# Performance work log

Measured on AMD Instinct MI355X. Metric: run time of the kernel, lower is better.

Reference implementation:

```python
import jax, jax.numpy as jnp
import numpy as np

N, CIN, COUT, K, CSTYLE, H, W = 8, 512, 512, 3, 512, 64, 64
EPS = 1e-8
SQRT2 = 2.0 ** 0.5


def setup_inputs() -> dict:
    key = jax.random.key(0)
    ks = jax.random.split(key, 5)
    return {
        "x": jax.random.normal(ks[0], (N, CIN, H, W), jnp.float32),
        "style": jax.random.normal(ks[1], (N, CSTYLE), jnp.float32),
        "noise": jax.random.normal(ks[2], (N, 1, H, W), jnp.float32),
        "conv_weight": jax.random.normal(ks[3], (1, COUT, CIN, K, K), jnp.float32),
        "mod_weight": jax.random.normal(ks[4], (CIN, CSTYLE), jnp.float32) / np.float32(np.sqrt(CSTYLE)),
        "mod_bias": jnp.ones((CIN,), jnp.float32),
        "noise_weight": jnp.zeros((1,), jnp.float32),
        "act_bias": jnp.zeros((COUT,), jnp.float32),
    }


def reference(x, style, noise, conv_weight, mod_weight, mod_bias, noise_weight, act_bias):
    n = x.shape[0]
    # style modulation: linear(style) -> per-sample per-in-channel scale (style_bias=0)
    s = style @ mod_weight.T + mod_bias                       # (n, cin)
    # modulate shared weight (1, cout, cin, k, k) -> (n, cout, cin, k, k)
    w = conv_weight * s[:, None, :, None, None]
    # demodulate
    demod = jax.lax.rsqrt(jnp.sum(w * w, axis=(2, 3, 4)) + EPS)  # (n, cout)
    w = w * demod[:, :, None, None, None]
    # grouped conv: groups = batch
    w = w.reshape(n * COUT, CIN, K, K)
    xg = x.reshape(1, n * CIN, H, W)
    out = jax.lax.conv_general_dilated(
        xg, w,
        window_strides=(1, 1),
        padding=[(K // 2, K // 2), (K // 2, K // 2)],
        dimension_numbers=("NCHW", "OIHW", "NCHW"),
        feature_group_count=n,
    )
    out = out.reshape(n, COUT, H, W) * SQRT2
    # noise injection (scalar weight, broadcast noise)
    out = out + noise_weight[0] * noise
    # fused bias + leaky relu (slope 0.2)
    out = jax.nn.leaky_relu(out + act_bias[None, :, None, None], negative_slope=0.2)
    return out
```

## Files before the change

kernel.cpp:

```cpp
#include <hip/hip_runtime.h>
#include <hip/hip_bf16.h>
#include <stdint.h>


typedef __attribute__((ext_vector_type(8))) short short8;
typedef __attribute__((ext_vector_type(4))) float f32x4;
typedef __attribute__((ext_vector_type(4))) unsigned int uint4v;
typedef __attribute__((ext_vector_type(2))) unsigned int uint2v;

__device__ __forceinline__ unsigned short f2bf(float f) {
  unsigned u = __builtin_bit_cast(unsigned, f);
  u += 0x7FFFu + ((u >> 16) & 1u);
  return (unsigned short)(u >> 16);
}

__device__ __forceinline__ void g2l16(const void* g, void* l) {
  __builtin_amdgcn_global_load_lds(
      (const __attribute__((address_space(1))) void*)g,
      (__attribute__((address_space(3))) void*)l, 16, 0, 0);
}

__global__ void k_pre(const float* __restrict__ style, const float* __restrict__ mw,
                      const float* __restrict__ mb, const float* __restrict__ cw,
                      float* __restrict__ s_out, float* __restrict__ wsq) {
  int t = threadIdx.x;
  int b = blockIdx.x;
  if (b < 1024) {
    int wid = b * 4 + (t >> 6);
    int lane = t & 63;
    int n = wid >> 9, ci = wid & 511;
    float sum = 0.f;
#pragma unroll
    for (int i = 0; i < 8; ++i) {
      int k = lane + i * 64;
      sum += style[n * 512 + k] * mw[ci * 512 + k];
    }
#pragma unroll
    for (int off = 32; off; off >>= 1) sum += __shfl_xor(sum, off, 64);
    if (lane == 0) s_out[wid] = sum + mb[ci];
  } else {
    int id = (b - 1024) * 256 + t;
    const float* p = cw + (size_t)id * 9;
    float a = 0.f;
#pragma unroll
    for (int j = 0; j < 9; ++j) a += p[j] * p[j];
    wsq[id] = a;
  }
}

__global__ void k_mid(const float* __restrict__ s, const float* __restrict__ wsq,
                      const float* __restrict__ x, const float* __restrict__ cw,
                      float* __restrict__ demod, unsigned short* __restrict__ Xp,
                      unsigned short* __restrict__ Wt) {
  __shared__ char smem[74240];
  int t = threadIdx.x;
  int b = blockIdx.x;
  if (b < 512) {
    int n = b >> 6, h = b & 63;
    short* ldsx = (short*)smem;
    float* sxf = (float*)(smem + 69632);
    sxf[t] = s[n * 512 + t];
    sxf[t + 256] = s[n * 512 + 256 + t];
    __syncthreads();
    const float* xb = x + ((size_t)n * 512) * 4096 + h * 64;
#pragma unroll
    for (int i = 0; i < 32; ++i) {
      int L = t + i * 256;
      int ci = L >> 4, q = L & 15;
      f32x4 v = *(const f32x4*)(xb + (size_t)ci * 4096 + q * 4);
      float sv = sxf[ci];
      uint2v o;
      o.x = f2bf(v.x * sv) | ((unsigned)f2bf(v.y * sv) << 16);
      o.y = f2bf(v.z * sv) | ((unsigned)f2bf(v.w * sv) << 16);
      *(uint2v*)(ldsx + ci * 68 + q * 4) = o;
    }
    __syncthreads();
    unsigned short* nb = Xp + (size_t)n * 2230272 + (size_t)(h + 1) * 33792;
#pragma unroll
    for (int r = 0; r < 16; ++r) {
      int u = t + r * 256;
      int cig = u >> 6, col = u & 63;
      unsigned v[8];
#pragma unroll
      for (int j = 0; j < 8; ++j)
        v[j] = (unsigned short)ldsx[(cig * 8 + j) * 68 + col];
      uint4v o;
      o.x = v[0] | (v[1] << 16);
      o.y = v[2] | (v[3] << 16);
      o.z = v[4] | (v[5] << 16);
      o.w = v[6] | (v[7] << 16);
      *(uint4v*)(nb + ((size_t)cig * 66 + col + 1) * 8) = o;
    }
  } else if (b < 1536) {
    int wid = (b - 512) * 4 + (t >> 6);
    int lane = t & 63;
    int n = wid >> 9, co = wid & 511;
    float sum = 0.f;
#pragma unroll
    for (int i = 0; i < 8; ++i) {
      int ci = lane + i * 64;
      float sv = s[n * 512 + ci];
      sum += sv * sv * wsq[co * 512 + ci];
    }
#pragma unroll
    for (int off = 32; off; off >>= 1) sum += __shfl_xor(sum, off, 64);
    if (lane == 0) demod[wid] = rsqrtf(sum + 1e-8f) * 1.41421356237309515f;
  } else if (b < 1792) {
    int bb = b - 1536;
    int cb = bb >> 4, kb = bb & 15;
    float* ldsf = (float*)smem;
#pragma unroll
    for (int i = 0; i < 36; ++i) {
      int idx = t + i * 256;
      int seg = idx / 288, off = idx - seg * 288;
      ldsf[seg * 289 + off] = cw[(size_t)(cb * 32 + seg) * 4608 + kb * 288 + off];
    }
    __syncthreads();
    unsigned short* ob = Wt + (size_t)(cb * 16 + kb) * 9216;
#pragma unroll
    for (int i = 0; i < 5; ++i) {
      int c = t + i * 256;
      if (c < 1152) {
        int m = c & 15, lhi = (c >> 4) & 3, mt = (c >> 6) & 1, tap = c >> 7;
        int co_rel = mt * 16 + m;
        unsigned v[8];
#pragma unroll
        for (int j = 0; j < 8; ++j)
          v[j] = f2bf(ldsf[co_rel * 289 + (lhi * 8 + j) * 9 + tap]);
        uint4v o;
        o.x = v[0] | (v[1] << 16);
        o.y = v[2] | (v[3] << 16);
        o.z = v[4] | (v[5] << 16);
        o.w = v[6] | (v[7] << 16);
        *(uint4v*)(ob + (size_t)c * 8) = o;
      }
    }
  } else {
    int bb = b - 1792;
    int n = bb / 17, part = bb % 17;
    uint4v z = (uint4v){0u, 0u, 0u, 0u};
    unsigned short* base = Xp + (size_t)n * 2230272;
#pragma unroll
    for (int i = 0; i < 4; ++i) {
      int id = part * 1024 + i * 256 + t;
      if (id < 16640) {
        size_t off;
        if (id < 8448) {
          int row = (id < 4224) ? 0 : 65;
          int c = id - ((id < 4224) ? 0 : 4224);
          off = (size_t)row * 33792 + (size_t)c * 8;
        } else {
          int id2 = id - 8448;
          int row = 1 + (id2 >> 7);
          int rem = id2 & 127;
          int klhi = rem >> 1;
          int col = (rem & 1) ? 65 : 0;
          off = (size_t)row * 33792 + ((size_t)klhi * 66 + col) * 8;
        }
        *(uint4v*)(base + off) = z;
      }
    }
  }
}

__global__ void __launch_bounds__(256, 3) k_conv(
    const unsigned short* __restrict__ Wt, const unsigned short* __restrict__ Xp,
    const float* __restrict__ demod, const float* __restrict__ noise,
    const float* __restrict__ nw_p, const float* __restrict__ act_bias,
    float* __restrict__ out) {
  __shared__ short lds_a[9216];
  __shared__ short lds_x[16896];
  int t = threadIdx.x;
  int bx = blockIdx.x;
  int r0 = (bx < 10) ? bx * 6 : 58;
  int cb = blockIdx.y;
  int n = blockIdx.z;
  int lane = t & 63, wv = t >> 6;
  int l15 = lane & 15, lhi4 = lane >> 4;

  const unsigned short* abase = Wt + (size_t)cb * 16 * 9216;
  const unsigned short* xbase = Xp + (size_t)n * 2230272;
  int xoffg[9];
#pragma unroll
  for (int j = 0; j < 9; ++j) {
    int c = j * 256 + t;
    int r = c / 264, rc = c - r * 264;
    int off = (r0 + r) * 33792 + rc * 8;
    if (c >= 2112) off = 0;
    xoffg[j] = off;
  }

  f32x4 acc[2][6];
#pragma unroll
  for (int a = 0; a < 2; ++a)
#pragma unroll
    for (int bq = 0; bq < 6; ++bq) acc[a][bq] = (f32x4){0.f, 0.f, 0.f, 0.f};

  const int aoff = lhi4 * 128 + l15 * 8;
  const int xoffb = lhi4 * 528 + (wv * 16 + l15) * 8;

  for (int kb = 0; kb < 16; ++kb) {
    __syncthreads();
    const char* ab = (const char*)(abase + (size_t)kb * 9216);
#pragma unroll
    for (int i = 0; i < 5; ++i) {
      int c = i * 256 + t;
      if (c < 1152) g2l16(ab + c * 16, (char*)lds_a + c * 16);
    }
#pragma unroll
    for (int j = 0; j < 9; ++j) {
      int c = j * 256 + t;
      if (c < 2112) g2l16(xbase + xoffg[j] + kb * 2112, (char*)lds_x + c * 16);
    }
    __syncthreads();

#pragma unroll
    for (int dw = 0; dw < 3; ++dw) {
      short8 bf[8];
#pragma unroll
      for (int rr = 0; rr < 8; ++rr)
        bf[rr] = *(const short8*)(lds_x + rr * 2112 + dw * 8 + xoffb);
#pragma unroll
      for (int dh = 0; dh < 3; ++dh) {
#pragma unroll
        for (int mt = 0; mt < 2; ++mt) {
          short8 af = *(const short8*)(lds_a + (dh * 3 + dw) * 1024 + mt * 512 + aoff);
#pragma unroll
          for (int ri = 0; ri < 6; ++ri)
            acc[mt][ri] =
                __builtin_amdgcn_mfma_f32_16x16x32_bf16(af, bf[ri + dh], acc[mt][ri], 0, 0, 0);
        }
      }
    }
  }

  float nw = nw_p[0];
  int col = wv * 16 + l15;
  float nz[6];
#pragma unroll
  for (int ri = 0; ri < 6; ++ri)
    nz[ri] = nw * noise[((size_t)n * 64 + r0 + ri) * 64 + col];
#pragma unroll
  for (int mt = 0; mt < 2; ++mt) {
    f32x4 dm4 = *(const f32x4*)(demod + n * 512 + cb * 32 + mt * 16 + lhi4 * 4);
#pragma unroll
    for (int c = 0; c < 4; ++c) {
      int co = cb * 32 + mt * 16 + lhi4 * 4 + c;
      float ab2 = act_bias[co];
      float dm = dm4[c];
#pragma unroll
      for (int ri = 0; ri < 6; ++ri) {
        float v = dm * acc[mt][ri][c] + nz[ri] + ab2;
        v = v > 0.f ? v : 0.2f * v;
        out[(((size_t)n * 512 + co) * 64 + (r0 + ri)) * 64 + col] = v;
      }
    }
  }
}

extern "C" void kernel_launch(void* const* d_in, const int* in_sizes, int n_in,
                              void* d_out, int out_size, void* d_ws, size_t ws_size,
                              hipStream_t stream) {
  const float* x     = (const float*)d_in[0];
  const float* style = (const float*)d_in[1];
  const float* noise = (const float*)d_in[2];
  const float* cw    = (const float*)d_in[3];
  const float* mw    = (const float*)d_in[4];
  const float* mb    = (const float*)d_in[5];
  const float* nw    = (const float*)d_in[6];
  const float* ab    = (const float*)d_in[7];
  float* out = (float*)d_out;

  char* ws = (char*)d_ws;
  float* s_buf  = (float*)ws;
  float* demod  = (float*)(ws + 16384);
  float* wsq    = (float*)(ws + 32768);
  unsigned short* Wt = (unsigned short*)(ws + 1081344);
  unsigned short* Xp = (unsigned short*)(ws + 5799936);

  k_pre<<<2048, 256, 0, stream>>>(style, mw, mb, cw, s_buf, wsq);
  k_mid<<<1928, 256, 0, stream>>>(s_buf, wsq, x, cw, demod, Xp, Wt);
  k_conv<<<dim3(11, 16, 8), 256, 0, stream>>>(Wt, Xp, demod, noise, nw, ab, out);
}
```

Before: 269.3 us.

## Switch conv inner loop to 32x32x16 MFMA with reworked weight layout

Replaces the 16x16x32 bf16 MFMA tiling with 32x32x16 MFMAs. The weight repack now stores 32 output channels contiguously per k-slice, and waves are split into column-halves and row-groups. This reduces the LDS operand loads per MFMA and raises arithmetic intensity per wave. The launch grid is also flattened to 1D with the batch index in the low bits, which changes workgroup ordering and likely L2 locality across samples. The cost is a different accumulator register footprint and epilogue store pattern.

```diff
diff --git a/kernel.cpp b/kernel.cpp
--- a/kernel.cpp
+++ b/kernel.cpp
@@ -5,6 +5,7 @@
 
 typedef __attribute__((ext_vector_type(8))) short short8;
 typedef __attribute__((ext_vector_type(4))) float f32x4;
+typedef __attribute__((ext_vector_type(16))) float f32x16;
 typedef __attribute__((ext_vector_type(4))) unsigned int uint4v;
 typedef __attribute__((ext_vector_type(2))) unsigned int uint2v;
 
@@ -121,8 +122,7 @@
     for (int i = 0; i < 5; ++i) {
       int c = t + i * 256;
       if (c < 1152) {
-        int m = c & 15, lhi = (c >> 4) & 3, mt = (c >> 6) & 1, tap = c >> 7;
-        int co_rel = mt * 16 + m;
+        int co_rel = c & 31, lhi = (c >> 5) & 3, tap = c >> 7;
         unsigned v[8];
 #pragma unroll
         for (int j = 0; j < 8; ++j)
@@ -171,12 +171,15 @@
   __shared__ short lds_a[9216];
   __shared__ short lds_x[16896];
   int t = threadIdx.x;
-  int bx = blockIdx.x;
+  int wg = blockIdx.x;
+  int n = wg & 7;
+  int rem = wg >> 3;
+  int cb = rem / 11;
+  int bx = rem - cb * 11;
   int r0 = (bx < 10) ? bx * 6 : 58;
-  int cb = blockIdx.y;
-  int n = blockIdx.z;
   int lane = t & 63, wv = t >> 6;
-  int l15 = lane & 15, lhi4 = lane >> 4;
+  int l31 = lane & 31, hi = lane >> 5;
+  int ch = wv >> 1, rg = wv & 1;
 
   const unsigned short* abase = Wt + (size_t)cb * 16 * 9216;
   const unsigned short* xbase = Xp + (size_t)n * 2230272;
@@ -190,14 +193,14 @@
     xoffg[j] = off;
   }
 
-  f32x4 acc[2][6];
-#pragma unroll
-  for (int a = 0; a < 2; ++a)
-#pragma unroll
-    for (int bq = 0; bq < 6; ++bq) acc[a][bq] = (f32x4){0.f, 0.f, 0.f, 0.f};
-
-  const int aoff = lhi4 * 128 + l15 * 8;
-  const int xoffb = lhi4 * 528 + (wv * 16 + l15) * 8;
+  f32x16 acc[3];
+#pragma unroll
+  for (int r = 0; r < 3; ++r)
+#pragma unroll
+    for (int q = 0; q < 16; ++q) acc[r][q] = 0.f;
+
+  const int aoff = hi * 256 + l31 * 8;
+  const int xb0 = hi * 528 + ch * 256 + l31 * 8;
 
   for (int kb = 0; kb < 16; ++kb) {
     __syncthreads();
@@ -216,43 +219,48 @@
 
 #pragma unroll
     for (int dw = 0; dw < 3; ++dw) {
-      short8 bf[8];
-#pragma unroll
-      for (int rr = 0; rr < 8; ++rr)
-        bf[rr] = *(const short8*)(lds_x + rr * 2112 + dw * 8 + xoffb);
+      short8 bf[5][2];
+#pragma unroll
+      for (int rr = 0; rr < 5; ++rr)
+#pragma unroll
+        for (int ks = 0; ks < 2; ++ks)
+          bf[rr][ks] = *(const short8*)(lds_x + (rg * 3 + rr) * 2112 + ks * 1056 +
+                                        dw * 8 + xb0);
 #pragma unroll
       for (int dh = 0; dh < 3; ++dh) {
-#pragma unroll
-        for (int mt = 0; mt < 2; ++mt) {
-          short8 af = *(const short8*)(lds_a + (dh * 3 + dw) * 1024 + mt * 512 + aoff);
-#pragma unroll
-          for (int ri = 0; ri < 6; ++ri)
-            acc[mt][ri] =
-                __builtin_amdgcn_mfma_f32_16x16x32_bf16(af, bf[ri + dh], acc[mt][ri], 0, 0, 0);
+        int tap = dh * 3 + dw;
+#pragma unroll
+        for (int ks = 0; ks < 2; ++ks) {
+          short8 af = *(const short8*)(lds_a + tap * 1024 + ks * 512 + aoff);
+#pragma unroll
+          for (int r = 0; r < 3; ++r)
+            acc[r] = __builtin_amdgcn_mfma_f32_32x32x16_bf16(af, bf[r + dh][ks],
+                                                             acc[r], 0, 0, 0);
         }
       }
     }
   }
 
   float nw = nw_p[0];
-  int col = wv * 16 + l15;
-  float nz[6];
-#pragma unroll
-  for (int ri = 0; ri < 6; ++ri)
-    nz[ri] = nw * noise[((size_t)n * 64 + r0 + ri) * 64 + col];
-#pragma unroll
-  for (int mt = 0; mt < 2; ++mt) {
-    f32x4 dm4 = *(const f32x4*)(demod + n * 512 + cb * 32 + mt * 16 + lhi4 * 4);
-#pragma unroll
-    for (int c = 0; c < 4; ++c) {
-      int co = cb * 32 + mt * 16 + lhi4 * 4 + c;
-      float ab2 = act_bias[co];
-      float dm = dm4[c];
-#pragma unroll
-      for (int ri = 0; ri < 6; ++ri) {
-        float v = dm * acc[mt][ri][c] + nz[ri] + ab2;
+  int col = ch * 32 + l31;
+  f32x4 dm4[4], ab4[4];
+#pragma unroll
+  for (int q = 0; q < 4; ++q) {
+    dm4[q] = *(const f32x4*)(demod + n * 512 + cb * 32 + q * 8 + hi * 4);
+    ab4[q] = *(const f32x4*)(act_bias + cb * 32 + q * 8 + hi * 4);
+  }
+#pragma unroll
+  for (int r = 0; r < 3; ++r) {
+    int R = r0 + rg * 3 + r;
+    float nz = nw * noise[((size_t)n * 64 + R) * 64 + col];
+#pragma unroll
+    for (int q = 0; q < 4; ++q) {
+#pragma unroll
+      for (int c = 0; c < 4; ++c) {
+        int co = cb * 32 + q * 8 + hi * 4 + c;
+        float v = dm4[q][c] * acc[r][q * 4 + c] + nz + ab4[q][c];
         v = v > 0.f ? v : 0.2f * v;
-        out[(((size_t)n * 512 + co) * 64 + (r0 + ri)) * 64 + col] = v;
+        out[(((size_t)n * 512 + co) * 64 + R) * 64 + col] = v;
       }
     }
   }
@@ -280,5 +288,5 @@
 
   k_pre<<<2048, 256, 0, stream>>>(style, mw, mb, cw, s_buf, wsq);
   k_mid<<<1928, 256, 0, stream>>>(s_buf, wsq, x, cw, demod, Xp, Wt);
-  k_conv<<<dim3(11, 16, 8), 256, 0, stream>>>(Wt, Xp, demod, noise, nw, ab, out);
-}
+  k_conv<<<1408, 256, 0, stream>>>(Wt, Xp, demod, noise, nw, ab, out);
+}
```

Result: no change. 270.0 us (+0.3%).
